# Kernel optimization log

Hardware: AMD Instinct MI355X
Metric: run time of the kernel (lower is better)

The kernel has to match this reference:

```python
import jax, jax.numpy as jnp
import numpy as np

M_PLUS, M_MINUS, LAMBDA = 0.9, 0.1, 0.5
NUM_CLASSES = 21
IGNORE = 255


def setup_inputs() -> dict:
    key = jax.random.key(0)
    k1, k2 = jax.random.split(key)
    class_caps = jax.random.normal(k1, (8, NUM_CLASSES, 16), dtype=jnp.float32)
    raw = jax.random.randint(k2, (8, 512, 512), 0, NUM_CLASSES + 1).astype(jnp.int32)
    # value NUM_CLASSES acts as the ignore label (255), exercising the ignore path
    labels = jnp.where(raw == NUM_CLASSES, IGNORE, raw).astype(jnp.int32)
    return {"class_caps": class_caps, "labels": labels}


def reference(class_caps, labels):
    B = class_caps.shape[0]
    C = NUM_CLASSES
    # capsule lengths: [B, C]
    caps_lengths = jnp.sqrt(jnp.sum(class_caps ** 2, axis=2))

    lbl = labels.reshape(B, -1)                       # [B, P]
    ignore = lbl == IGNORE
    lbl_clean = jnp.where(ignore, 0, lbl)
    valid = (~ignore).astype(jnp.float32)

    # image-level multi-label presence: max over valid pixels of one-hot labels,
    # done as a scatter-max instead of materializing a [B, P, C] one-hot tensor.
    bidx = jnp.broadcast_to(jnp.arange(B)[:, None], lbl.shape)
    image_labels = jnp.zeros((B, C), jnp.float32).at[bidx, lbl_clean].max(valid)

    left = jax.nn.relu(M_PLUS - caps_lengths) ** 2
    right = jax.nn.relu(caps_lengths - M_MINUS) ** 2
    margin = image_labels * left + LAMBDA * (1.0 - image_labels) * right
    margin_loss = jnp.mean(jnp.sum(margin, axis=1))

    margin_loss_weight = 1.0
    total_loss = margin_loss_weight * margin_loss
    return total_loss
```

## Files before the change

kernel.cpp:

```cpp
#include <hip/hip_runtime.h>
#include <hip/hip_bf16.h>

#define NC 21
#define LAMBDA 0.5f

#define SIG  0x2B3u
#define SIGW (SIG << 21)
#define SENT 0x80000000u

__global__ __launch_bounds__(256) void caps_fused(
        const int* __restrict__ labels, const float* __restrict__ caps,
        unsigned* bm, float* __restrict__ out) {
    int t = threadIdx.x;
    if (blockIdx.x < 256) {
        const int4* L = reinterpret_cast<const int4*>(labels)
                        + (size_t)blockIdx.x * 2048;
        unsigned m = 0;
        #pragma unroll
        for (int k = 0; k < 8; ++k) {
            int4 v = L[t + k * 256];
            if ((unsigned)v.x < (unsigned)NC) m |= 1u << v.x;
            if ((unsigned)v.y < (unsigned)NC) m |= 1u << v.y;
            if ((unsigned)v.z < (unsigned)NC) m |= 1u << v.z;
            if ((unsigned)v.w < (unsigned)NC) m |= 1u << v.w;
        }
        #pragma unroll
        for (int s = 1; s < 64; s <<= 1) m |= __shfl_xor(m, s, 64);
        if ((t & 63) == 0)
            atomicExch(bm + blockIdx.x * 4 + (t >> 6), m | SIGW);
        return;
    }

    float l = 0.0f, r = 0.0f;
    if (t < 8 * NC) {
        const float* p = caps + t * 16;
        float s2 = 0.0f;
        #pragma unroll
        for (int d = 0; d < 16; ++d) { float x = p[d]; s2 += x * x; }
        float len = sqrtf(s2);
        l = fmaxf(0.9f - len, 0.0f);  l *= l;
        r = fmaxf(len - 0.1f, 0.0f);  r *= r;
    }

    unsigned acc = 0, got = 0;
    unsigned* base = bm + t * 4;
    while (got != 0xFu) {
        #pragma unroll
        for (int k = 0; k < 4; ++k) {
            if (!(got & (1u << k))) {
                unsigned v = atomicExch(base + k, SENT);
                if ((v >> 21) == SIG) { acc |= v & 0x1FFFFFu; got |= 1u << k; }
            }
        }
        if (got != 0xFu) __builtin_amdgcn_s_sleep(1);
    }

    #pragma unroll
    for (int s = 16; s; s >>= 1) acc |= __shfl_xor(acc, s, 64);
    __shared__ unsigned pres[8];
    __shared__ float psum[4];
    if ((t & 31) == 0) pres[t >> 5] = acc;
    __syncthreads();

    float v = 0.0f;
    if (t < 8 * NC) {
        int bb = t / NC, c = t % NC;
        v = ((pres[bb] >> c) & 1u) ? l : LAMBDA * r;
    }
    #pragma unroll
    for (int s = 32; s; s >>= 1) v += __shfl_xor(v, s, 64);
    if ((t & 63) == 0) psum[t >> 6] = v;
    __syncthreads();
    if (t == 0) out[0] = (psum[0] + psum[1] + psum[2] + psum[3]) * 0.125f;
}

extern "C" void kernel_launch(void* const* d_in, const int* in_sizes, int n_in,
                              void* d_out, int out_size, void* d_ws, size_t ws_size,
                              hipStream_t stream) {
    const float* caps   = (const float*)d_in[0];
    const int*   labels = (const int*)d_in[1];
    float* out = (float*)d_out;
    unsigned* bm = (unsigned*)d_ws;

    caps_fused<<<257, 256, 0, stream>>>(labels, caps, bm, out);
}
```

Measured before the change: 11.65 us.

## Replace dedicated reducer block with last-arriving-wave ticket finalization

Drops the extra 257th spin-waiting block. Each wave now publishes its label bitmask and takes a ticket with a wrapping atomicInc, and the wave that draws the winning ticket gathers all 1024 masks and computes the loss. Every block also computes capsule lengths redundantly, loading them as float4, so the finishing wave already holds them. This removes the reducer block that could spin while occupying a CU. The cost is an extra atomic per wave plus redundant caps loads, and the winning wave may still spin until every mask is visible.

```diff
diff --git a/kernel.cpp b/kernel.cpp
--- a/kernel.cpp
+++ b/kernel.cpp
@@ -4,74 +4,89 @@
 #define NC 21
 #define LAMBDA 0.5f
 
-#define SIG  0x2B3u
-#define SIGW (SIG << 21)
-#define SENT 0x80000000u
+#define SIG   0x2B3u
+#define SIGW  (SIG << 21)
+#define SENT  0x80000000u
 
-__global__ __launch_bounds__(256) void caps_fused(
+#define TICKET_WIN 1022u
+
+__global__ __launch_bounds__(256) void caps_one(
         const int* __restrict__ labels, const float* __restrict__ caps,
-        unsigned* bm, float* __restrict__ out) {
+        unsigned* bm, unsigned* ticket, float* __restrict__ out) {
     int t = threadIdx.x;
-    if (blockIdx.x < 256) {
-        const int4* L = reinterpret_cast<const int4*>(labels)
-                        + (size_t)blockIdx.x * 2048;
-        unsigned m = 0;
-        #pragma unroll
-        for (int k = 0; k < 8; ++k) {
-            int4 v = L[t + k * 256];
-            if ((unsigned)v.x < (unsigned)NC) m |= 1u << v.x;
-            if ((unsigned)v.y < (unsigned)NC) m |= 1u << v.y;
-            if ((unsigned)v.z < (unsigned)NC) m |= 1u << v.z;
-            if ((unsigned)v.w < (unsigned)NC) m |= 1u << v.w;
-        }
-        #pragma unroll
-        for (int s = 1; s < 64; s <<= 1) m |= __shfl_xor(m, s, 64);
-        if ((t & 63) == 0)
-            atomicExch(bm + blockIdx.x * 4 + (t >> 6), m | SIGW);
-        return;
+    int lane = t & 63;
+
+    const int4* L = reinterpret_cast<const int4*>(labels)
+                    + (size_t)blockIdx.x * 2048;
+    unsigned m = 0;
+    #pragma unroll
+    for (int k = 0; k < 8; ++k) {
+        int4 v = L[t + k * 256];
+        if ((unsigned)v.x < (unsigned)NC) m |= 1u << v.x;
+        if ((unsigned)v.y < (unsigned)NC) m |= 1u << v.y;
+        if ((unsigned)v.z < (unsigned)NC) m |= 1u << v.z;
+        if ((unsigned)v.w < (unsigned)NC) m |= 1u << v.w;
     }
 
-    float l = 0.0f, r = 0.0f;
-    if (t < 8 * NC) {
-        const float* p = caps + t * 16;
-        float s2 = 0.0f;
-        #pragma unroll
-        for (int d = 0; d < 16; ++d) { float x = p[d]; s2 += x * x; }
-        float len = sqrtf(s2);
-        l = fmaxf(0.9f - len, 0.0f);  l *= l;
-        r = fmaxf(len - 0.1f, 0.0f);  r *= r;
+    float lv[3] = {0.f, 0.f, 0.f}, rv[3] = {0.f, 0.f, 0.f};
+    #pragma unroll
+    for (int k = 0; k < 3; ++k) {
+        int idx = lane + k * 64;
+        if (idx < 8 * NC) {
+            const float4* p = reinterpret_cast<const float4*>(caps + idx * 16);
+            float4 a = p[0], b4 = p[1], c4 = p[2], d4 = p[3];
+            float s2 = a.x*a.x + a.y*a.y + a.z*a.z + a.w*a.w
+                     + b4.x*b4.x + b4.y*b4.y + b4.z*b4.z + b4.w*b4.w
+                     + c4.x*c4.x + c4.y*c4.y + c4.z*c4.z + c4.w*c4.w
+                     + d4.x*d4.x + d4.y*d4.y + d4.z*d4.z + d4.w*d4.w;
+            float len = sqrtf(s2);
+            float l = fmaxf(0.9f - len, 0.f);  lv[k] = l * l;
+            float r = fmaxf(len - 0.1f, 0.f);  rv[k] = r * r;
+        }
     }
 
-    unsigned acc = 0, got = 0;
-    unsigned* base = bm + t * 4;
-    while (got != 0xFu) {
+    #pragma unroll
+    for (int s = 1; s < 64; s <<= 1) m |= __shfl_xor(m, s, 64);
+    int slot = blockIdx.x * 4 + (t >> 6);
+    unsigned old = 0;
+    if (lane == 0) {
+        atomicExch(bm + slot, m | SIGW);
+        old = atomicInc(ticket, 1023u);
+    }
+    old = __shfl(old, 0, 64);
+    if (old != TICKET_WIN) return;
+
+    unsigned acc = 0;
+    unsigned got = 0;
+    unsigned* base = bm + lane * 16;
+    while (got != 0xFFFFu) {
         #pragma unroll
-        for (int k = 0; k < 4; ++k) {
+        for (int k = 0; k < 16; ++k) {
             if (!(got & (1u << k))) {
                 unsigned v = atomicExch(base + k, SENT);
                 if ((v >> 21) == SIG) { acc |= v & 0x1FFFFFu; got |= 1u << k; }
             }
         }
-        if (got != 0xFu) __builtin_amdgcn_s_sleep(1);
-    }
-
-    #pragma unroll
-    for (int s = 16; s; s >>= 1) acc |= __shfl_xor(acc, s, 64);
-    __shared__ unsigned pres[8];
-    __shared__ float psum[4];
-    if ((t & 31) == 0) pres[t >> 5] = acc;
-    __syncthreads();
-
-    float v = 0.0f;
-    if (t < 8 * NC) {
-        int bb = t / NC, c = t % NC;
-        v = ((pres[bb] >> c) & 1u) ? l : LAMBDA * r;
+        if (got != 0xFFFFu) __builtin_amdgcn_s_sleep(1);
     }
     #pragma unroll
-    for (int s = 32; s; s >>= 1) v += __shfl_xor(v, s, 64);
-    if ((t & 63) == 0) psum[t >> 6] = v;
-    __syncthreads();
-    if (t == 0) out[0] = (psum[0] + psum[1] + psum[2] + psum[3]) * 0.125f;
+    for (int s = 1; s < 8; s <<= 1) acc |= __shfl_xor(acc, s, 64);
+
+    float sum = 0.f;
+    #pragma unroll
+    for (int k = 0; k < 3; ++k) {
+        int idx = lane + k * 64;
+        int valid = idx < 8 * NC;
+        int bb = valid ? idx / NC : 0;
+        unsigned pb = __shfl(acc, bb << 3, 64);
+        if (valid) {
+            int c = idx - bb * NC;
+            sum += ((pb >> c) & 1u) ? lv[k] : LAMBDA * rv[k];
+        }
+    }
+    #pragma unroll
+    for (int s = 1; s < 64; s <<= 1) sum += __shfl_xor(sum, s, 64);
+    if (lane == 0) out[0] = sum * 0.125f;
 }
 
 extern "C" void kernel_launch(void* const* d_in, const int* in_sizes, int n_in,
@@ -81,6 +96,7 @@
     const int*   labels = (const int*)d_in[1];
     float* out = (float*)d_out;
     unsigned* bm = (unsigned*)d_ws;
+    unsigned* ticket = (unsigned*)((char*)d_ws + 4096);
 
-    caps_fused<<<257, 256, 0, stream>>>(labels, caps, bm, out);
+    caps_one<<<256, 256, 0, stream>>>(labels, caps, bm, ticket, out);
 }
```

Measured after the change: 25.95 us. +122.7%, slower.

## Merge finalizer into block 0 and reduce per-block masks via shared memory

Applied to the files above, without the earlier changes.

Drops the separate 257th finalizer block: block 0 now computes capsule lengths, scans its own share of labels, then spins on all 256 per-block masks. Each block ORs its four wave masks through shared memory and publishes a single word, so the finalizer polls 256 words with one per thread instead of four. This cuts atomic traffic and polling work, and the capsule loads become float4. The cost is that block 0 does label work before it starts waiting, and correctness relies on all 256 blocks being resident at the same time.

```diff
diff --git a/kernel.cpp b/kernel.cpp
--- a/kernel.cpp
+++ b/kernel.cpp
@@ -4,72 +4,73 @@
 #define NC 21
 #define LAMBDA 0.5f
 
-#define SIG  0x2B3u
-#define SIGW (SIG << 21)
-#define SENT 0x80000000u
+#define SIG   0x2B3u
+#define SIGW  (SIG << 21)
+#define SENT  0x80000000u
 
-__global__ __launch_bounds__(256) void caps_fused(
+__global__ __launch_bounds__(256) void caps_one(
         const int* __restrict__ labels, const float* __restrict__ caps,
         unsigned* bm, float* __restrict__ out) {
     int t = threadIdx.x;
-    if (blockIdx.x < 256) {
-        const int4* L = reinterpret_cast<const int4*>(labels)
-                        + (size_t)blockIdx.x * 2048;
-        unsigned m = 0;
-        #pragma unroll
-        for (int k = 0; k < 8; ++k) {
-            int4 v = L[t + k * 256];
-            if ((unsigned)v.x < (unsigned)NC) m |= 1u << v.x;
-            if ((unsigned)v.y < (unsigned)NC) m |= 1u << v.y;
-            if ((unsigned)v.z < (unsigned)NC) m |= 1u << v.z;
-            if ((unsigned)v.w < (unsigned)NC) m |= 1u << v.w;
-        }
-        #pragma unroll
-        for (int s = 1; s < 64; s <<= 1) m |= __shfl_xor(m, s, 64);
-        if ((t & 63) == 0)
-            atomicExch(bm + blockIdx.x * 4 + (t >> 6), m | SIGW);
-        return;
+    int lane = t & 63;
+    bool isb0 = blockIdx.x == 0;
+
+    __shared__ unsigned wm[4];
+    __shared__ unsigned pres[8];
+    __shared__ float psum[4];
+
+    float lterm = 0.f, rterm = 0.f;
+    if (isb0 && t < 8 * NC) {
+        const float4* p = reinterpret_cast<const float4*>(caps + t * 16);
+        float4 a = p[0], b4 = p[1], c4 = p[2], d4 = p[3];
+        float s2 = a.x*a.x + a.y*a.y + a.z*a.z + a.w*a.w
+                 + b4.x*b4.x + b4.y*b4.y + b4.z*b4.z + b4.w*b4.w
+                 + c4.x*c4.x + c4.y*c4.y + c4.z*c4.z + c4.w*c4.w
+                 + d4.x*d4.x + d4.y*d4.y + d4.z*d4.z + d4.w*d4.w;
+        float len = sqrtf(s2);
+        float l = fmaxf(0.9f - len, 0.f);  lterm = l * l;
+        float r = fmaxf(len - 0.1f, 0.f);  rterm = r * r;
     }
 
-    float l = 0.0f, r = 0.0f;
-    if (t < 8 * NC) {
-        const float* p = caps + t * 16;
-        float s2 = 0.0f;
-        #pragma unroll
-        for (int d = 0; d < 16; ++d) { float x = p[d]; s2 += x * x; }
-        float len = sqrtf(s2);
-        l = fmaxf(0.9f - len, 0.0f);  l *= l;
-        r = fmaxf(len - 0.1f, 0.0f);  r *= r;
+    const int4* L = reinterpret_cast<const int4*>(labels)
+                    + (size_t)blockIdx.x * 2048;
+    unsigned m = 0;
+    #pragma unroll
+    for (int k = 0; k < 8; ++k) {
+        int4 v = L[t + k * 256];
+        if ((unsigned)v.x < (unsigned)NC) m |= 1u << v.x;
+        if ((unsigned)v.y < (unsigned)NC) m |= 1u << v.y;
+        if ((unsigned)v.z < (unsigned)NC) m |= 1u << v.z;
+        if ((unsigned)v.w < (unsigned)NC) m |= 1u << v.w;
     }
+    #pragma unroll
+    for (int s = 1; s < 64; s <<= 1) m |= __shfl_xor(m, s, 64);
+    if (lane == 0) wm[t >> 6] = m;
+    __syncthreads();
+    if (t == 0)
+        atomicExch(bm + blockIdx.x, (wm[0] | wm[1] | wm[2] | wm[3]) | SIGW);
+    if (!isb0) return;
 
-    unsigned acc = 0, got = 0;
-    unsigned* base = bm + t * 4;
-    while (got != 0xFu) {
-        #pragma unroll
-        for (int k = 0; k < 4; ++k) {
-            if (!(got & (1u << k))) {
-                unsigned v = atomicExch(base + k, SENT);
-                if ((v >> 21) == SIG) { acc |= v & 0x1FFFFFu; got |= 1u << k; }
-            }
-        }
-        if (got != 0xFu) __builtin_amdgcn_s_sleep(1);
+    unsigned v;
+    for (;;) {
+        v = atomicExch(bm + t, SENT);
+        if ((v >> 21) == SIG) break;
+        __builtin_amdgcn_s_sleep(1);
     }
-
+    unsigned acc = v & 0x1FFFFFu;
     #pragma unroll
     for (int s = 16; s; s >>= 1) acc |= __shfl_xor(acc, s, 64);
-    __shared__ unsigned pres[8];
-    __shared__ float psum[4];
     if ((t & 31) == 0) pres[t >> 5] = acc;
     __syncthreads();
 
-    float v = 0.0f;
+    float val = 0.f;
     if (t < 8 * NC) {
-        int bb = t / NC, c = t % NC;
-        v = ((pres[bb] >> c) & 1u) ? l : LAMBDA * r;
+        int bb = t / NC, c = t - bb * NC;
+        val = ((pres[bb] >> c) & 1u) ? lterm : LAMBDA * rterm;
     }
     #pragma unroll
-    for (int s = 32; s; s >>= 1) v += __shfl_xor(v, s, 64);
-    if ((t & 63) == 0) psum[t >> 6] = v;
+    for (int s = 32; s; s >>= 1) val += __shfl_xor(val, s, 64);
+    if (lane == 0) psum[t >> 6] = val;
     __syncthreads();
     if (t == 0) out[0] = (psum[0] + psum[1] + psum[2] + psum[3]) * 0.125f;
 }
@@ -82,5 +83,5 @@
     float* out = (float*)d_out;
     unsigned* bm = (unsigned*)d_ws;
 
-    caps_fused<<<257, 256, 0, stream>>>(labels, caps, bm, out);
+    caps_one<<<256, 256, 0, stream>>>(labels, caps, bm, out);
 }
```

Measured after the change: 9.738 us. -16.4%, faster.
